# Kernel optimization log

Measured on AMD Instinct MI355X. Metric: run time of the kernel, lower is better.

The kernel has to match this reference:

```python
import jax, jax.numpy as jnp
import numpy as np

B = 65536
X_DIM = 362
A = 3  # action_space / number of expert dynamics MLPs


def setup_inputs() -> dict:
    key = jax.random.key(0)
    ks = jax.random.split(key, 12)
    batch_x = jax.random.normal(ks[0], (B, X_DIM), dtype=jnp.float32)
    batch_next = jax.random.normal(ks[1], (B, X_DIM), dtype=jnp.float32)
    # Plant the pointer sentinel (value 10.0) at a random in-bounds grid cell per row,
    # so that ptr-19 >= 0 and ptr+19 < X_DIM (grid width is 19).
    ptr_pos = jax.random.randint(ks[2], (B,), 20, 343)
    batch_x = batch_x.at[jnp.arange(B), ptr_pos].set(10.0)
    batch_a = jax.random.randint(ks[3], (B,), 0, A, dtype=jnp.int32)

    def lin(k, fan_in, shape):
        return (jax.random.normal(k, shape, dtype=jnp.float32) / np.sqrt(fan_in)).astype(jnp.float32)

    W1 = lin(ks[4], 6, (A, 6, 100));   b1 = jnp.zeros((A, 100), jnp.float32)
    W2 = lin(ks[5], 100, (A, 100, 400)); b2 = jnp.zeros((A, 400), jnp.float32)
    W3 = lin(ks[6], 400, (A, 400, 100)); b3 = jnp.zeros((A, 100), jnp.float32)
    W4 = lin(ks[7], 100, (A, 100, 6));  b4 = jnp.zeros((A, 6), jnp.float32)
    return {"batch_x": batch_x, "batch_next": batch_next, "batch_a": batch_a,
            "W1": W1, "b1": b1, "W2": W2, "b2": b2, "W3": W3, "b3": b3, "W4": W4, "b4": b4}


def _attend(data, ptr):
    # cell_list = [0, p, p-19 (left), p+19 (right), p-1 (above), p+1 (below)]
    zeros = jnp.zeros_like(ptr)
    idx = jnp.stack([zeros, ptr, ptr - 19, ptr + 19, ptr - 1, ptr + 1], axis=1)  # [B, 6]
    return jnp.take_along_axis(data, idx, axis=1)  # [B, 6]


def _expert(x, a, W1, b1, W2, b2, W3, b3, W4, b4):
    h = jax.nn.relu(x @ W1[a] + b1[a])
    h = jax.nn.relu(h @ W2[a] + b2[a])
    h = jax.nn.relu(h @ W3[a] + b3[a])
    return h @ W4[a] + b4[a]


def reference(batch_x, batch_next, batch_a, W1, b1, W2, b2, W3, b3, W4, b4):
    # Pointer index = first occurrence of sentinel value 10.0 per row.
    ptr = jnp.argmax(batch_x == 10.0, axis=1)  # [B]
    att = _attend(batch_x, ptr)        # [B, 6]
    att_next = _attend(batch_next, ptr)  # [B, 6]
    # Per-action routed expert MLPs (A is small and fixed): compute each expert
    # over the batch and select per-sample by action id.
    preds = jnp.zeros_like(att)
    for a in range(A):
        out_a = _expert(att, a, W1, b1, W2, b2, W3, b3, W4, b4)
        preds = jnp.where((batch_a == a)[:, None], out_a, preds)
    actual_deltas = att_next - att
    return jnp.mean((preds - actual_deltas) ** 2)
```

## Files before the change

kernel.cpp:

```cpp
#include <hip/hip_runtime.h>
#include <hip/hip_bf16.h>

#define B_ROWS 65536
#define XD 362

typedef __bf16 bf16;
typedef __attribute__((ext_vector_type(8))) __bf16 bf16x8;
typedef __attribute__((ext_vector_type(4))) float f32x4;
typedef __attribute__((ext_vector_type(2))) float f32x2;

#define MFMA16(A, Bf, C) __builtin_amdgcn_mfma_f32_16x16x32_bf16(A, Bf, C, 0, 0, 0)
#define ORDER() __builtin_amdgcn_sched_barrier(0x7F)

#define OFF_W1T   0u
#define OFF_W2T   21504u
#define OFF_W3T   340992u
#define OFF_W4T   620544u
#define OFF_CNT   632832u
#define OFF_PTR   633088u
#define OFF_ATTC  895232u
#define OFF_DELTA 4040960u
#define OFF_PART  8759552u

#define MLP_GRID 520
#define WPREP_BLOCKS 624
#define SCAN_BLOCKS 2896


__global__ __launch_bounds__(256) void k_prep(
    const float* __restrict__ W1, const float* __restrict__ b1,
    const float* __restrict__ W2, const float* __restrict__ b2,
    const float* __restrict__ W3, const float* __restrict__ b3,
    const float* __restrict__ W4, const float* __restrict__ b4,
    const float* __restrict__ x,
    bf16* __restrict__ W1t, bf16* __restrict__ W2t,
    bf16* __restrict__ W3t, bf16* __restrict__ W4t,
    int* __restrict__ cnt, int* __restrict__ ptrArr)
{
  int bx = blockIdx.x;
  if (bx >= WPREP_BLOCKS) {
    int gid = (bx - WPREP_BLOCKS) * 256 + threadIdx.x;
    const float4* x4 = (const float4*)x;
#pragma unroll
    for (int u = 0; u < 8; ++u) {
      int i = gid + u * (SCAN_BLOCKS * 256);
      float4 v = x4[i];
      if (v.x == 10.0f || v.y == 10.0f || v.z == 10.0f || v.w == 10.0f) {
        int flat = i * 4;
        if (v.x == 10.0f) ptrArr[(flat    ) / XD] = (flat    ) % XD;
        if (v.y == 10.0f) ptrArr[(flat + 1) / XD] = (flat + 1) % XD;
        if (v.z == 10.0f) ptrArr[(flat + 2) / XD] = (flat + 2) % XD;
        if (v.w == 10.0f) ptrArr[(flat + 3) / XD] = (flat + 3) % XD;
      }
    }
    return;
  }
  int i = bx * 256 + threadIdx.x;
  if (i == 0) { cnt[0] = 0; cnt[1] = 0; cnt[2] = 0; }
  if (i < 3*416*128) {
    int e = i & 7; int g = (i >> 3) & 15;
    int rn = i >> 7; int n = rn % 416; int a = rn / 416;
    int k = ((g ^ (n & 7)) << 3) | e;
    float v = 0.f;
    if (n < 400) {
      if (k < 100) v = W2[(a*100 + k)*400 + n];
      else if (k == 100) v = b2[a*400 + n];
    } else if (n == 400) {
      v = (k == 100) ? 1.0f : 0.0f;
    }
    W2t[i] = (bf16)v;
  }
  if (i < 3*13*112*32) {
    int e = i & 7; int g = (i >> 3) & 3;
    int n = (i >> 5) % 112; int tc = ((i >> 5) / 112) % 13; int a = i / (13*112*32);
    int k = tc * 32 + ((g ^ (n & 3)) << 3) + e;
    float v = 0.f;
    if (n < 100) {
      if (k < 400) v = W3[(a*400 + k)*100 + n];
      else if (k == 400) v = b3[a*100 + n];
    }
    W3t[i] = (bf16)v;
  }
  if (i < 3*112*32) {
    int k = i & 31; int rn = i >> 5; int n = rn % 112; int a = rn / 112;
    float v = 0.f;
    if (n < 100) {
      if (k < 6) v = W1[(a*6 + k)*100 + n];
      else if (k == 6) v = b1[a*100 + n];
    }
    W1t[i] = (bf16)v;
  }
  if (i < 3*16*128) {
    int k = i & 127; int rn = i >> 7; int n = rn & 15; int a = rn >> 4;
    float v = 0.f;
    if (n < 6) {
      if (k < 100) v = W4[(a*100 + k)*6 + n];
      else if (k == 100) v = b4[a*6 + n];
    }
    W4t[i] = (bf16)v;
  }
}

__global__ __launch_bounds__(256) void k_gather2(
    const float* __restrict__ x, const float* __restrict__ xn,
    const int* __restrict__ act, const int* __restrict__ ptrArr,
    bf16* __restrict__ attC, float* __restrict__ deltaC, int* __restrict__ cnt)
{
  int row = blockIdx.x * 256 + threadIdx.x;
  int lane = threadIdx.x & 63;
  int p = ptrArr[row];
  if (p < 20 || p > 342) p = 20;
  const float* xr = x  + (size_t)row * XD;
  const float* nr = xn + (size_t)row * XD;
  int cells[6] = {0, p, p - 19, p + 19, p - 1, p + 1};
  float av[6], dv[6];
#pragma unroll
  for (int i = 0; i < 6; ++i) {
    av[i] = xr[cells[i]];
    dv[i] = nr[cells[i]] - av[i];
  }
  int a = act[row];
  unsigned long long m0 = __ballot(a == 0);
  unsigned long long m1 = __ballot(a == 1);
  unsigned long long m2 = __ballot(a == 2);
  int b0 = 0, b1 = 0, b2 = 0;
  if (lane == 0) {
    b0 = atomicAdd(&cnt[0], (int)__popcll(m0));
    b1 = atomicAdd(&cnt[1], (int)__popcll(m1));
    b2 = atomicAdd(&cnt[2], (int)__popcll(m2));
  }
  b0 = __shfl(b0, 0); b1 = __shfl(b1, 0); b2 = __shfl(b2, 0);
  unsigned long long lt = (1ull << lane) - 1ull;
  unsigned long long ma = (a == 0) ? m0 : (a == 1) ? m1 : m2;
  int base            = (a == 0) ? b0 : (a == 1) ? b1 : b2;
  int slot = base + (int)__popcll(ma & lt);
  size_t rb = (size_t)a * B_ROWS + slot;
  bf16x8 av8;
#pragma unroll
  for (int i = 0; i < 6; ++i) av8[i] = (bf16)av[i];
  av8[6] = (bf16)1.0f;
  av8[7] = (bf16)0.0f;
  *(bf16x8*)(attC + rb * 8) = av8;
  f32x2 d01 = {dv[0], dv[1]}, d23 = {dv[2], dv[3]}, d45 = {dv[4], dv[5]};
  *(f32x2*)(deltaC + rb * 6)     = d01;
  *(f32x2*)(deltaC + rb * 6 + 2) = d23;
  *(f32x2*)(deltaC + rb * 6 + 4) = d45;
}

__global__ __launch_bounds__(256, 2) void k_mlp(
    const bf16* __restrict__ W1t, const bf16* __restrict__ W2t,
    const bf16* __restrict__ W3t, const bf16* __restrict__ W4t,
    const bf16* __restrict__ attC, const float* __restrict__ deltaC,
    const int* __restrict__ cnt, float* __restrict__ partial)
{
  int c0 = cnt[0], c1 = cnt[1], c2 = cnt[2];
  int T0 = (c0 + 127) >> 7, T1 = (c1 + 127) >> 7, T2 = (c2 + 127) >> 7;
  int b = blockIdx.x;
  int a, tile, count;
  if (b < T0)           { a = 0; tile = b;            count = c0; }
  else if (b < T0 + T1) { a = 1; tile = b - T0;       count = c1; }
  else if (b < T0 + T1 + T2) { a = 2; tile = b - T0 - T1; count = c2; }
  else { if (threadIdx.x == 0) partial[b] = 0.f; return; }
  int start = tile << 7;

  __shared__ __align__(16) bf16 bufW2[3][32][128];
  __shared__ __align__(16) bf16 bufW3[3][112][32];
  __shared__ __align__(16) bf16 dummyLds[512];
  __shared__ __align__(16) bf16 h1s[4][16][136];
  __shared__ __align__(16) bf16 tr[4][2][16][56];
  __shared__ float s_part[4];
  int wv = threadIdx.x >> 6, lane = threadIdx.x & 63;
  int q = lane >> 4, c = lane & 15;
  int cx7 = c & 7, cx3 = c & 3;

  const bf16* W1a = W1t + a * 112 * 32;
  const bf16* W2a = W2t + a * 416 * 128;
  const bf16* W3a = W3t + a * 13 * 112 * 32;
  const bf16* W4a = W4t + a * 16 * 128;

  auto stage = [&](int tn) {
    int sl = tn % 3;
    const char* s2 = (const char*)W2a + tn * 8192;
    const char* s3 = (const char*)W3a + tn * 7168;
    char* d2 = (char*)&bufW2[sl][0][0];
    char* d3 = (char*)&bufW3[sl][0][0];
#pragma unroll
    for (int r = 0; r < 4; ++r) {
      int id = wv + r * 4;
      const char* src;
      char* dst;
      if (id < 8)       { src = s2 + id * 1024 + lane * 16;       dst = d2 + id * 1024; }
      else if (id < 15) { src = s3 + (id - 8) * 1024 + lane * 16; dst = d3 + (id - 8) * 1024; }
      else              { src = s3 + 6 * 1024 + lane * 16;        dst = (char*)&dummyLds[0]; }
      __builtin_amdgcn_global_load_lds(
          (const __attribute__((address_space(1))) unsigned int*)src,
          (__attribute__((address_space(3))) unsigned int*)dst, 16, 0, 0);
    }
  };

  stage(0);

  for (int i = lane; i < 16 * 16; i += 64)
    h1s[wv][i >> 4][112 + (i & 15)] = (bf16)0.0f;

  bf16x8 A2[2][4];
#pragma unroll
  for (int mi = 0; mi < 2; ++mi) {
    bf16x8 aAtt;
#pragma unroll
    for (int i = 0; i < 8; ++i) aAtt[i] = (bf16)0.0f;
    int slot = start + wv * 32 + mi * 16 + c;
    if (q == 0 && slot < count)
      aAtt = *(const bf16x8*)(attC + ((size_t)a * B_ROWS + slot) * 8);
#pragma unroll
    for (int nt = 0; nt < 7; ++nt) {
      bf16x8 bw = *(const bf16x8*)(W1a + (nt * 16 + c) * 32 + q * 8);
      f32x4 C = {0.f, 0.f, 0.f, 0.f};
      C = MFMA16(aAtt, bw, C);
      int n = nt * 16 + c;
#pragma unroll
      for (int rg = 0; rg < 4; ++rg) {
        float v = (n < 100) ? (C[rg] > 0.f ? C[rg] : 0.f)
                            : (n == 100 ? 1.0f : 0.0f);
        h1s[wv][q * 4 + rg][n] = (bf16)v;
      }
    }
    ORDER();
#pragma unroll
    for (int tt = 0; tt < 4; ++tt)
      A2[mi][tt] = *(const bf16x8*)&h1s[wv][c][tt * 32 + q * 8];
    ORDER();
  }

  f32x4 C3[2][7];
#pragma unroll
  for (int mi = 0; mi < 2; ++mi)
#pragma unroll
    for (int i = 0; i < 7; ++i) C3[mi][i] = (f32x4){0.f, 0.f, 0.f, 0.f};

#pragma unroll 1
  for (int t = 0; t < 13; ++t) {
    if (t < 12) {
      stage(t + 1);
      asm volatile("s_waitcnt vmcnt(4)" ::: "memory");
    } else {
      asm volatile("s_waitcnt vmcnt(0)" ::: "memory");
    }
    __builtin_amdgcn_s_barrier();
    __builtin_amdgcn_sched_barrier(0);

    int sl = t % 3;
    const bf16* cw2 = &bufW2[sl][0][0];
    const bf16* cw3 = &bufW3[sl][0][0];
    bf16x8 w3f[7];
#pragma unroll
    for (int nt3 = 0; nt3 < 7; ++nt3)
      w3f[nt3] = *(const bf16x8*)(cw3 + (nt3 * 16 + c) * 32 + ((q ^ cx3) << 3));
    bf16x8 b2f[2][4];
#pragma unroll
    for (int half = 0; half < 2; ++half)
#pragma unroll
      for (int tt = 0; tt < 4; ++tt)
        b2f[half][tt] = *(const bf16x8*)(cw2 + (half * 16 + c) * 128 +
                                         ((((tt << 2) + q) ^ cx7) << 3));

#pragma unroll
    for (int mi = 0; mi < 2; ++mi)
#pragma unroll
      for (int half = 0; half < 2; ++half) {
        f32x4 C = {0.f, 0.f, 0.f, 0.f};
#pragma unroll
        for (int tt = 0; tt < 4; ++tt)
          C = MFMA16(A2[mi][tt], b2f[half][tt], C);
#pragma unroll
        for (int rg = 0; rg < 4; ++rg) {
          float v = C[rg] > 0.f ? C[rg] : 0.f;
          tr[wv][mi][q * 4 + rg][half * 16 + c] = (bf16)v;
        }
      }
    ORDER();
    bf16x8 A3a = *(const bf16x8*)&tr[wv][0][c][q * 8];
    bf16x8 A3b = *(const bf16x8*)&tr[wv][1][c][q * 8];
#pragma unroll
    for (int nt3 = 0; nt3 < 7; ++nt3) {
      C3[0][nt3] = MFMA16(A3a, w3f[nt3], C3[0][nt3]);
      C3[1][nt3] = MFMA16(A3b, w3f[nt3], C3[1][nt3]);
    }
    ORDER();
    asm volatile("s_waitcnt lgkmcnt(0)" ::: "memory");
    __builtin_amdgcn_sched_barrier(0);
  }

  bf16x8 b4f[4];
#pragma unroll
  for (int tt = 0; tt < 4; ++tt)
    b4f[tt] = *(const bf16x8*)(W4a + c * 128 + tt * 32 + q * 8);
  float sq = 0.f;
#pragma unroll
  for (int mi = 0; mi < 2; ++mi) {
#pragma unroll
    for (int nt3 = 0; nt3 < 7; ++nt3) {
      int n = nt3 * 16 + c;
#pragma unroll
      for (int rg = 0; rg < 4; ++rg) {
        float v = (n < 100) ? (C3[mi][nt3][rg] > 0.f ? C3[mi][nt3][rg] : 0.f)
                            : (n == 100 ? 1.0f : 0.0f);
        h1s[wv][q * 4 + rg][n] = (bf16)v;
      }
    }
    ORDER();
    f32x4 C4 = {0.f, 0.f, 0.f, 0.f};
#pragma unroll
    for (int tt = 0; tt < 4; ++tt) {
      bf16x8 A4 = *(const bf16x8*)&h1s[wv][c][tt * 32 + q * 8];
      C4 = MFMA16(A4, b4f[tt], C4);
    }
    ORDER();
    if (c < 6) {
#pragma unroll
      for (int rg = 0; rg < 4; ++rg) {
        int slot = start + wv * 32 + mi * 16 + q * 4 + rg;
        if (slot < count) {
          float d = deltaC[((size_t)a * B_ROWS + slot) * 6 + c];
          float e = C4[rg] - d;
          sq += e * e;
        }
      }
    }
  }
#pragma unroll
  for (int off = 32; off; off >>= 1) sq += __shfl_xor(sq, off);
  if (lane == 0) s_part[wv] = sq;
  __syncthreads();
  if (threadIdx.x == 0)
    partial[b] = s_part[0] + s_part[1] + s_part[2] + s_part[3];
}

__global__ __launch_bounds__(256) void k_final(
    const float* __restrict__ partial, float* __restrict__ out)
{
  __shared__ float s[4];
  int t = threadIdx.x, lane = t & 63, wv = t >> 6;
  float sum = 0.f;
  for (int i = t; i < MLP_GRID; i += 256) sum += partial[i];
#pragma unroll
  for (int off = 32; off; off >>= 1) sum += __shfl_xor(sum, off);
  if (lane == 0) s[wv] = sum;
  __syncthreads();
  if (t == 0) {
    double tot = (double)s[0] + s[1] + s[2] + s[3];
    out[0] = (float)(tot / (double)(B_ROWS * 6));
  }
}

extern "C" void kernel_launch(void* const* d_in, const int* in_sizes, int n_in,
                              void* d_out, int out_size, void* d_ws, size_t ws_size,
                              hipStream_t stream)
{
  const float* x  = (const float*)d_in[0];
  const float* xn = (const float*)d_in[1];
  const int*  act = (const int*)d_in[2];
  const float* W1 = (const float*)d_in[3];
  const float* b1 = (const float*)d_in[4];
  const float* W2 = (const float*)d_in[5];
  const float* b2 = (const float*)d_in[6];
  const float* W3 = (const float*)d_in[7];
  const float* b3 = (const float*)d_in[8];
  const float* W4 = (const float*)d_in[9];
  const float* b4 = (const float*)d_in[10];

  char* ws = (char*)d_ws;
  bf16*   W1t    = (bf16*)(ws + OFF_W1T);
  bf16*   W2t    = (bf16*)(ws + OFF_W2T);
  bf16*   W3t    = (bf16*)(ws + OFF_W3T);
  bf16*   W4t    = (bf16*)(ws + OFF_W4T);
  int*    cnt    = (int*)(ws + OFF_CNT);
  int*    ptrArr = (int*)(ws + OFF_PTR);
  bf16*   attC   = (bf16*)(ws + OFF_ATTC);
  float*  deltaC = (float*)(ws + OFF_DELTA);
  float*  part   = (float*)(ws + OFF_PART);

  k_prep<<<dim3(WPREP_BLOCKS + SCAN_BLOCKS), dim3(256), 0, stream>>>(
      W1, b1, W2, b2, W3, b3, W4, b4, x, W1t, W2t, W3t, W4t, cnt, ptrArr);
  k_gather2<<<dim3(B_ROWS / 256), dim3(256), 0, stream>>>(x, xn, act, ptrArr,
                                                          attC, deltaC, cnt);
  k_mlp<<<dim3(MLP_GRID), dim3(256), 0, stream>>>(W1t, W2t, W3t, W4t,
                                                  attC, deltaC, cnt, part);
  k_final<<<dim3(1), dim3(256), 0, stream>>>(part, (float*)d_out);
}
```

Measured before the change: 272.7 us.

## Software-pipeline layer-2/3 MFMA chunks with double-buffered transposed h2 staging

Restructures the fused layer-2/layer-3 loop so that the layer-3 MFMAs for the previous chunk run alongside the layer-2 MFMAs for the current chunk. W3 fragments are carried across iterations in registers. The operand order of the MFMAs is swapped so results come out transposed, which lets the h2 and h3 activations be written to shared memory as packed 4-wide bf16 stores instead of scalar stores. Weight staging drops from triple to double buffering with a full vmcnt(0) wait plus barrier each iteration, and the MFMA section runs under raised wave priority (s_setprio). The aim is to remove the serial store, barrier and reload bubble between the layers, at the cost of more live registers and tighter load/compute overlap.

```diff
diff --git a/kernel.cpp b/kernel.cpp
--- a/kernel.cpp
+++ b/kernel.cpp
@@ -6,6 +6,7 @@
 
 typedef __bf16 bf16;
 typedef __attribute__((ext_vector_type(8))) __bf16 bf16x8;
+typedef __attribute__((ext_vector_type(4))) __bf16 bf16x4;
 typedef __attribute__((ext_vector_type(4))) float f32x4;
 typedef __attribute__((ext_vector_type(2))) float f32x2;
 
@@ -163,11 +164,11 @@
   else { if (threadIdx.x == 0) partial[b] = 0.f; return; }
   int start = tile << 7;
 
-  __shared__ __align__(16) bf16 bufW2[3][32][128];
-  __shared__ __align__(16) bf16 bufW3[3][112][32];
+  __shared__ __align__(16) bf16 bufW2[2][32][128];
+  __shared__ __align__(16) bf16 bufW3[2][112][32];
   __shared__ __align__(16) bf16 dummyLds[512];
   __shared__ __align__(16) bf16 h1s[4][16][136];
-  __shared__ __align__(16) bf16 tr[4][2][16][56];
+  __shared__ __align__(16) bf16 h2ch[4][2][2][16][40];
   __shared__ float s_part[4];
   int wv = threadIdx.x >> 6, lane = threadIdx.x & 63;
   int q = lane >> 4, c = lane & 15;
@@ -179,7 +180,7 @@
   const bf16* W4a = W4t + a * 16 * 128;
 
   auto stage = [&](int tn) {
-    int sl = tn % 3;
+    int sl = tn & 1;
     const char* s2 = (const char*)W2a + tn * 8192;
     const char* s3 = (const char*)W3a + tn * 7168;
     char* d2 = (char*)&bufW2[sl][0][0];
@@ -238,24 +239,18 @@
 #pragma unroll
     for (int i = 0; i < 7; ++i) C3[mi][i] = (f32x4){0.f, 0.f, 0.f, 0.f};
 
-#pragma unroll 1
-  for (int t = 0; t < 13; ++t) {
-    if (t < 12) {
-      stage(t + 1);
-      asm volatile("s_waitcnt vmcnt(4)" ::: "memory");
-    } else {
-      asm volatile("s_waitcnt vmcnt(0)" ::: "memory");
-    }
-    __builtin_amdgcn_s_barrier();
-    __builtin_amdgcn_sched_barrier(0);
-
-    int sl = t % 3;
-    const bf16* cw2 = &bufW2[sl][0][0];
-    const bf16* cw3 = &bufW3[sl][0][0];
-    bf16x8 w3f[7];
+  bf16x8 w3fP[7];
+
+  asm volatile("s_waitcnt vmcnt(0)" ::: "memory");
+  __builtin_amdgcn_s_barrier();
+  __builtin_amdgcn_sched_barrier(0);
+  stage(1);
+  {
+    const bf16* cw2 = &bufW2[0][0][0];
+    const bf16* cw3 = &bufW3[0][0][0];
 #pragma unroll
     for (int nt3 = 0; nt3 < 7; ++nt3)
-      w3f[nt3] = *(const bf16x8*)(cw3 + (nt3 * 16 + c) * 32 + ((q ^ cx3) << 3));
+      w3fP[nt3] = *(const bf16x8*)(cw3 + (nt3 * 16 + c) * 32 + ((q ^ cx3) << 3));
     bf16x8 b2f[2][4];
 #pragma unroll
     for (int half = 0; half < 2; ++half)
@@ -263,7 +258,8 @@
       for (int tt = 0; tt < 4; ++tt)
         b2f[half][tt] = *(const bf16x8*)(cw2 + (half * 16 + c) * 128 +
                                          ((((tt << 2) + q) ^ cx7) << 3));
-
+    __builtin_amdgcn_sched_barrier(0);
+    __builtin_amdgcn_s_setprio(1);
 #pragma unroll
     for (int mi = 0; mi < 2; ++mi)
 #pragma unroll
@@ -271,24 +267,79 @@
         f32x4 C = {0.f, 0.f, 0.f, 0.f};
 #pragma unroll
         for (int tt = 0; tt < 4; ++tt)
-          C = MFMA16(A2[mi][tt], b2f[half][tt], C);
-#pragma unroll
-        for (int rg = 0; rg < 4; ++rg) {
-          float v = C[rg] > 0.f ? C[rg] : 0.f;
-          tr[wv][mi][q * 4 + rg][half * 16 + c] = (bf16)v;
-        }
-      }
-    ORDER();
-    bf16x8 A3a = *(const bf16x8*)&tr[wv][0][c][q * 8];
-    bf16x8 A3b = *(const bf16x8*)&tr[wv][1][c][q * 8];
-#pragma unroll
-    for (int nt3 = 0; nt3 < 7; ++nt3) {
-      C3[0][nt3] = MFMA16(A3a, w3f[nt3], C3[0][nt3]);
-      C3[1][nt3] = MFMA16(A3b, w3f[nt3], C3[1][nt3]);
-    }
-    ORDER();
+          C = MFMA16(b2f[half][tt], A2[mi][tt], C);
+        bf16x4 pk;
+#pragma unroll
+        for (int rg = 0; rg < 4; ++rg)
+          pk[rg] = (bf16)(C[rg] > 0.f ? C[rg] : 0.f);
+        *(bf16x4*)&h2ch[wv][0][mi][c][half * 16 + q * 4] = pk;
+      }
+    __builtin_amdgcn_s_setprio(0);
     asm volatile("s_waitcnt lgkmcnt(0)" ::: "memory");
     __builtin_amdgcn_sched_barrier(0);
+  }
+
+#pragma unroll 1
+  for (int t = 1; t < 13; ++t) {
+    asm volatile("s_waitcnt vmcnt(0)" ::: "memory");
+    __builtin_amdgcn_s_barrier();
+    __builtin_amdgcn_sched_barrier(0);
+    if (t < 12) stage(t + 1);
+    const bf16* cw2 = &bufW2[t & 1][0][0];
+    const bf16* cw3 = &bufW3[t & 1][0][0];
+    bf16x8 A3[2];
+#pragma unroll
+    for (int mi = 0; mi < 2; ++mi)
+      A3[mi] = *(const bf16x8*)&h2ch[wv][(t - 1) & 1][mi][c][q * 8];
+    bf16x8 w3fN[7];
+#pragma unroll
+    for (int nt3 = 0; nt3 < 7; ++nt3)
+      w3fN[nt3] = *(const bf16x8*)(cw3 + (nt3 * 16 + c) * 32 + ((q ^ cx3) << 3));
+    bf16x8 b2f[2][4];
+#pragma unroll
+    for (int half = 0; half < 2; ++half)
+#pragma unroll
+      for (int tt = 0; tt < 4; ++tt)
+        b2f[half][tt] = *(const bf16x8*)(cw2 + (half * 16 + c) * 128 +
+                                         ((((tt << 2) + q) ^ cx7) << 3));
+    __builtin_amdgcn_sched_barrier(0);
+    __builtin_amdgcn_s_setprio(1);
+#pragma unroll
+    for (int nt3 = 0; nt3 < 7; ++nt3) {
+      C3[0][nt3] = MFMA16(w3fP[nt3], A3[0], C3[0][nt3]);
+      C3[1][nt3] = MFMA16(w3fP[nt3], A3[1], C3[1][nt3]);
+    }
+#pragma unroll
+    for (int mi = 0; mi < 2; ++mi)
+#pragma unroll
+      for (int half = 0; half < 2; ++half) {
+        f32x4 C = {0.f, 0.f, 0.f, 0.f};
+#pragma unroll
+        for (int tt = 0; tt < 4; ++tt)
+          C = MFMA16(b2f[half][tt], A2[mi][tt], C);
+        bf16x4 pk;
+#pragma unroll
+        for (int rg = 0; rg < 4; ++rg)
+          pk[rg] = (bf16)(C[rg] > 0.f ? C[rg] : 0.f);
+        *(bf16x4*)&h2ch[wv][t & 1][mi][c][half * 16 + q * 4] = pk;
+      }
+    __builtin_amdgcn_s_setprio(0);
+#pragma unroll
+    for (int nt3 = 0; nt3 < 7; ++nt3) w3fP[nt3] = w3fN[nt3];
+    asm volatile("s_waitcnt lgkmcnt(0)" ::: "memory");
+    __builtin_amdgcn_sched_barrier(0);
+  }
+
+  {
+    bf16x8 A3[2];
+#pragma unroll
+    for (int mi = 0; mi < 2; ++mi)
+      A3[mi] = *(const bf16x8*)&h2ch[wv][0][mi][c][q * 8];
+#pragma unroll
+    for (int nt3 = 0; nt3 < 7; ++nt3) {
+      C3[0][nt3] = MFMA16(w3fP[nt3], A3[0], C3[0][nt3]);
+      C3[1][nt3] = MFMA16(w3fP[nt3], A3[1], C3[1][nt3]);
+    }
   }
 
   bf16x8 b4f[4];
@@ -300,13 +351,15 @@
   for (int mi = 0; mi < 2; ++mi) {
 #pragma unroll
     for (int nt3 = 0; nt3 < 7; ++nt3) {
-      int n = nt3 * 16 + c;
+      bf16x4 pk;
 #pragma unroll
       for (int rg = 0; rg < 4; ++rg) {
-        float v = (n < 100) ? (C3[mi][nt3][rg] > 0.f ? C3[mi][nt3][rg] : 0.f)
-                            : (n == 100 ? 1.0f : 0.0f);
-        h1s[wv][q * 4 + rg][n] = (bf16)v;
-      }
+        int k3 = nt3 * 16 + q * 4 + rg;
+        float v = (k3 < 100) ? (C3[mi][nt3][rg] > 0.f ? C3[mi][nt3][rg] : 0.f)
+                             : (k3 == 100 ? 1.0f : 0.0f);
+        pk[rg] = (bf16)v;
+      }
+      *(bf16x4*)&h1s[wv][c][nt3 * 16 + q * 4] = pk;
     }
     ORDER();
     f32x4 C4 = {0.f, 0.f, 0.f, 0.f};
```

Measured after the change: 268.1 us. No clear change (-1.7%).

## Double the MLP block to 512 threads and restage weights via transposed MFMA

Applied to the files above, without the earlier changes.

The MLP kernel now uses 512-thread blocks covering 256 rows each, with half the grid. Each block stages the shared W2/W3 weight chunk once for twice as many rows, and the staging buffer drops from triple to double buffering. The MFMA operands are swapped so each lane produces contiguous packed bf16x4 writes into a per-wave LDS pool that is reused for the layer-1, layer-2 and layer-3 activations. s_setprio is raised around the MFMA section. The aim is to cut weight-load traffic per row and LDS write overhead, at the cost of more LDS pressure per block, a tighter barrier-then-prefetch schedule and fewer blocks for load balancing.

```diff
diff --git a/kernel.cpp b/kernel.cpp
--- a/kernel.cpp
+++ b/kernel.cpp
@@ -6,6 +6,7 @@
 
 typedef __bf16 bf16;
 typedef __attribute__((ext_vector_type(8))) __bf16 bf16x8;
+typedef __attribute__((ext_vector_type(4))) __bf16 bf16x4;
 typedef __attribute__((ext_vector_type(4))) float f32x4;
 typedef __attribute__((ext_vector_type(2))) float f32x2;
 
@@ -22,7 +23,7 @@
 #define OFF_DELTA 4040960u
 #define OFF_PART  8759552u
 
-#define MLP_GRID 520
+#define MLP_GRID 264
 #define WPREP_BLOCKS 624
 #define SCAN_BLOCKS 2896
 
@@ -147,31 +148,32 @@
   *(f32x2*)(deltaC + rb * 6 + 4) = d45;
 }
 
-__global__ __launch_bounds__(256, 2) void k_mlp(
+__global__ __launch_bounds__(512, 4) void k_mlp(
     const bf16* __restrict__ W1t, const bf16* __restrict__ W2t,
     const bf16* __restrict__ W3t, const bf16* __restrict__ W4t,
     const bf16* __restrict__ attC, const float* __restrict__ deltaC,
     const int* __restrict__ cnt, float* __restrict__ partial)
 {
   int c0 = cnt[0], c1 = cnt[1], c2 = cnt[2];
-  int T0 = (c0 + 127) >> 7, T1 = (c1 + 127) >> 7, T2 = (c2 + 127) >> 7;
+  int T0 = (c0 + 255) >> 8, T1 = (c1 + 255) >> 8, T2 = (c2 + 255) >> 8;
   int b = blockIdx.x;
   int a, tile, count;
   if (b < T0)           { a = 0; tile = b;            count = c0; }
   else if (b < T0 + T1) { a = 1; tile = b - T0;       count = c1; }
   else if (b < T0 + T1 + T2) { a = 2; tile = b - T0 - T1; count = c2; }
   else { if (threadIdx.x == 0) partial[b] = 0.f; return; }
-  int start = tile << 7;
-
-  __shared__ __align__(16) bf16 bufW2[3][32][128];
-  __shared__ __align__(16) bf16 bufW3[3][112][32];
+  int start = tile << 8;
+
+  __shared__ __align__(16) bf16 bufW2[2][32][128];
+  __shared__ __align__(16) bf16 bufW3[2][112][32];
   __shared__ __align__(16) bf16 dummyLds[512];
-  __shared__ __align__(16) bf16 h1s[4][16][136];
-  __shared__ __align__(16) bf16 tr[4][2][16][56];
-  __shared__ float s_part[4];
+  __shared__ __align__(16) char pool[8][4608];
+  __shared__ float s_part[8];
   int wv = threadIdx.x >> 6, lane = threadIdx.x & 63;
   int q = lane >> 4, c = lane & 15;
   int cx7 = c & 7, cx3 = c & 3;
+  bf16 (*h1s)[136]    = (bf16(*)[136])   &pool[wv][0];
+  bf16 (*h2c)[16][40] = (bf16(*)[16][40])&pool[wv][0];
 
   const bf16* W1a = W1t + a * 112 * 32;
   const bf16* W2a = W2t + a * 416 * 128;
@@ -179,14 +181,14 @@
   const bf16* W4a = W4t + a * 16 * 128;
 
   auto stage = [&](int tn) {
-    int sl = tn % 3;
+    int sl = tn & 1;
     const char* s2 = (const char*)W2a + tn * 8192;
     const char* s3 = (const char*)W3a + tn * 7168;
     char* d2 = (char*)&bufW2[sl][0][0];
     char* d3 = (char*)&bufW3[sl][0][0];
 #pragma unroll
-    for (int r = 0; r < 4; ++r) {
-      int id = wv + r * 4;
+    for (int r = 0; r < 2; ++r) {
+      int id = wv + r * 8;
       const char* src;
       char* dst;
       if (id < 8)       { src = s2 + id * 1024 + lane * 16;       dst = d2 + id * 1024; }
@@ -201,7 +203,7 @@
   stage(0);
 
   for (int i = lane; i < 16 * 16; i += 64)
-    h1s[wv][i >> 4][112 + (i & 15)] = (bf16)0.0f;
+    h1s[i >> 4][112 + (i & 15)] = (bf16)0.0f;
 
   bf16x8 A2[2][4];
 #pragma unroll
@@ -222,13 +224,13 @@
       for (int rg = 0; rg < 4; ++rg) {
         float v = (n < 100) ? (C[rg] > 0.f ? C[rg] : 0.f)
                             : (n == 100 ? 1.0f : 0.0f);
-        h1s[wv][q * 4 + rg][n] = (bf16)v;
+        h1s[q * 4 + rg][n] = (bf16)v;
       }
     }
     ORDER();
 #pragma unroll
     for (int tt = 0; tt < 4; ++tt)
-      A2[mi][tt] = *(const bf16x8*)&h1s[wv][c][tt * 32 + q * 8];
+      A2[mi][tt] = *(const bf16x8*)&h1s[c][tt * 32 + q * 8];
     ORDER();
   }
 
@@ -237,21 +239,17 @@
   for (int mi = 0; mi < 2; ++mi)
 #pragma unroll
     for (int i = 0; i < 7; ++i) C3[mi][i] = (f32x4){0.f, 0.f, 0.f, 0.f};
+
+  ORDER();
 
 #pragma unroll 1
   for (int t = 0; t < 13; ++t) {
-    if (t < 12) {
-      stage(t + 1);
-      asm volatile("s_waitcnt vmcnt(4)" ::: "memory");
-    } else {
-      asm volatile("s_waitcnt vmcnt(0)" ::: "memory");
-    }
+    asm volatile("s_waitcnt vmcnt(0)" ::: "memory");
     __builtin_amdgcn_s_barrier();
     __builtin_amdgcn_sched_barrier(0);
-
-    int sl = t % 3;
-    const bf16* cw2 = &bufW2[sl][0][0];
-    const bf16* cw3 = &bufW3[sl][0][0];
+    if (t < 12) stage(t + 1);
+    const bf16* cw2 = &bufW2[t & 1][0][0];
+    const bf16* cw3 = &bufW3[t & 1][0][0];
     bf16x8 w3f[7];
 #pragma unroll
     for (int nt3 = 0; nt3 < 7; ++nt3)
@@ -263,7 +261,8 @@
       for (int tt = 0; tt < 4; ++tt)
         b2f[half][tt] = *(const bf16x8*)(cw2 + (half * 16 + c) * 128 +
                                          ((((tt << 2) + q) ^ cx7) << 3));
-
+    __builtin_amdgcn_sched_barrier(0);
+    __builtin_amdgcn_s_setprio(1);
 #pragma unroll
     for (int mi = 0; mi < 2; ++mi)
 #pragma unroll
@@ -271,26 +270,28 @@
         f32x4 C = {0.f, 0.f, 0.f, 0.f};
 #pragma unroll
         for (int tt = 0; tt < 4; ++tt)
-          C = MFMA16(A2[mi][tt], b2f[half][tt], C);
-#pragma unroll
-        for (int rg = 0; rg < 4; ++rg) {
-          float v = C[rg] > 0.f ? C[rg] : 0.f;
-          tr[wv][mi][q * 4 + rg][half * 16 + c] = (bf16)v;
-        }
-      }
-    ORDER();
-    bf16x8 A3a = *(const bf16x8*)&tr[wv][0][c][q * 8];
-    bf16x8 A3b = *(const bf16x8*)&tr[wv][1][c][q * 8];
+          C = MFMA16(b2f[half][tt], A2[mi][tt], C);
+        bf16x4 pk;
+#pragma unroll
+        for (int rg = 0; rg < 4; ++rg)
+          pk[rg] = (bf16)(C[rg] > 0.f ? C[rg] : 0.f);
+        *(bf16x4*)&h2c[mi][c][half * 16 + q * 4] = pk;
+      }
+    ORDER();
+    bf16x8 A3a = *(const bf16x8*)&h2c[0][c][q * 8];
+    bf16x8 A3b = *(const bf16x8*)&h2c[1][c][q * 8];
 #pragma unroll
     for (int nt3 = 0; nt3 < 7; ++nt3) {
-      C3[0][nt3] = MFMA16(A3a, w3f[nt3], C3[0][nt3]);
-      C3[1][nt3] = MFMA16(A3b, w3f[nt3], C3[1][nt3]);
-    }
-    ORDER();
+      C3[0][nt3] = MFMA16(w3f[nt3], A3a, C3[0][nt3]);
+      C3[1][nt3] = MFMA16(w3f[nt3], A3b, C3[1][nt3]);
+    }
+    __builtin_amdgcn_s_setprio(0);
     asm volatile("s_waitcnt lgkmcnt(0)" ::: "memory");
     __builtin_amdgcn_sched_barrier(0);
   }
 
+  for (int i = lane; i < 16 * 16; i += 64)
+    h1s[i >> 4][112 + (i & 15)] = (bf16)0.0f;
   bf16x8 b4f[4];
 #pragma unroll
   for (int tt = 0; tt < 4; ++tt)
@@ -300,19 +301,21 @@
   for (int mi = 0; mi < 2; ++mi) {
 #pragma unroll
     for (int nt3 = 0; nt3 < 7; ++nt3) {
-      int n = nt3 * 16 + c;
+      bf16x4 pk;
 #pragma unroll
       for (int rg = 0; rg < 4; ++rg) {
-        float v = (n < 100) ? (C3[mi][nt3][rg] > 0.f ? C3[mi][nt3][rg] : 0.f)
-                            : (n == 100 ? 1.0f : 0.0f);
-        h1s[wv][q * 4 + rg][n] = (bf16)v;
-      }
+        int k3 = nt3 * 16 + q * 4 + rg;
+        float v = (k3 < 100) ? (C3[mi][nt3][rg] > 0.f ? C3[mi][nt3][rg] : 0.f)
+                             : (k3 == 100 ? 1.0f : 0.0f);
+        pk[rg] = (bf16)v;
+      }
+      *(bf16x4*)&h1s[c][nt3 * 16 + q * 4] = pk;
     }
     ORDER();
     f32x4 C4 = {0.f, 0.f, 0.f, 0.f};
 #pragma unroll
     for (int tt = 0; tt < 4; ++tt) {
-      bf16x8 A4 = *(const bf16x8*)&h1s[wv][c][tt * 32 + q * 8];
+      bf16x8 A4 = *(const bf16x8*)&h1s[c][tt * 32 + q * 8];
       C4 = MFMA16(A4, b4f[tt], C4);
     }
     ORDER();
@@ -332,8 +335,12 @@
   for (int off = 32; off; off >>= 1) sq += __shfl_xor(sq, off);
   if (lane == 0) s_part[wv] = sq;
   __syncthreads();
-  if (threadIdx.x == 0)
-    partial[b] = s_part[0] + s_part[1] + s_part[2] + s_part[3];
+  if (threadIdx.x == 0) {
+    float tot = 0.f;
+#pragma unroll
+    for (int w = 0; w < 8; ++w) tot += s_part[w];
+    partial[b] = tot;
+  }
 }
 
 __global__ __launch_bounds__(256) void k_final(
@@ -384,7 +391,7 @@
       W1, b1, W2, b2, W3, b3, W4, b4, x, W1t, W2t, W3t, W4t, cnt, ptrArr);
   k_gather2<<<dim3(B_ROWS / 256), dim3(256), 0, stream>>>(x, xn, act, ptrArr,
                                                           attC, deltaC, cnt);
-  k_mlp<<<dim3(MLP_GRID), dim3(256), 0, stream>>>(W1t, W2t, W3t, W4t,
+  k_mlp<<<dim3(MLP_GRID), dim3(512), 0, stream>>>(W1t, W2t, W3t, W4t,
                                                   attC, deltaC, cnt, part);
   k_final<<<dim3(1), dim3(256), 0, stream>>>(part, (float*)d_out);
 }
```

Measured after the change: 382.3 us. 40.2% more time.
